# Kernel optimization log

Measured on AMD Instinct MI355X. Metric: run time of the kernel, lower is better.

Reference implementation:

```python
import jax, jax.numpy as jnp
import numpy as np

NUM_HEADS = 8
HEAD_SPLITS = [2, 3, 3]            # heads per crpe window {3:2, 5:3, 7:3}
WINDOWS = [3, 5, 7]


def dwconv(x, w, b, pad):
    """Depthwise conv. x: [B,C,H,W], w: [C,1,kh,kw] (OIHW), b: [C]."""
    y = jax.lax.conv_general_dilated(
        x, w, window_strides=(1, 1), padding=[(pad, pad), (pad, pad)],
        dimension_numbers=("NCHW", "OIHW", "NCHW"),
        feature_group_count=x.shape[1])
    return y + b[None, :, None, None]


def layernorm(x, w, b, eps=1e-6):
    m = jnp.mean(x, axis=-1, keepdims=True)
    v = jnp.mean(jnp.square(x - m), axis=-1, keepdims=True)
    return (x - m) * jax.lax.rsqrt(v + eps) * w + b


def setup_inputs() -> dict:
    key = jax.random.key(0)
    ks = jax.random.split(key, 16)
    B, Hs, Ws, C = 16, 56, 56, 512
    N = Hs * Ws
    Ch = C // NUM_HEADS
    hid = int(C * 4.0)

    def rn(k, shape, s=0.02):
        return jax.random.normal(k, shape, jnp.float32) * s

    return {
        "x": jax.random.normal(ks[0], (B, N, C), jnp.float32),
        "H": Hs, "W": Ws,
        "cpe_w": rn(ks[1], (C, 1, 3, 3)), "cpe_b": jnp.zeros((C,), jnp.float32),
        "ln1_w": jnp.ones((C,), jnp.float32), "ln1_b": jnp.zeros((C,), jnp.float32),
        "qkv_w": rn(ks[2], (C, 3 * C)),
        "proj_w": rn(ks[3], (C, C)), "proj_b": jnp.zeros((C,), jnp.float32),
        "w3": rn(ks[4], (HEAD_SPLITS[0] * Ch, 1, 3, 3)), "b3": jnp.zeros((HEAD_SPLITS[0] * Ch,), jnp.float32),
        "w5": rn(ks[5], (HEAD_SPLITS[1] * Ch, 1, 5, 5)), "b5": jnp.zeros((HEAD_SPLITS[1] * Ch,), jnp.float32),
        "w7": rn(ks[6], (HEAD_SPLITS[2] * Ch, 1, 7, 7)), "b7": jnp.zeros((HEAD_SPLITS[2] * Ch,), jnp.float32),
        "ln2_w": jnp.ones((C,), jnp.float32), "ln2_b": jnp.zeros((C,), jnp.float32),
        "fc1_w": rn(ks[7], (C, hid)), "fc1_b": jnp.zeros((hid,), jnp.float32),
        "fc2_w": rn(ks[8], (hid, C)), "fc2_b": jnp.zeros((C,), jnp.float32),
    }


def reference(x, H, W, cpe_w, cpe_b, ln1_w, ln1_b, qkv_w, proj_w, proj_b,
              w3, b3, w5, b5, w7, b7, ln2_w, ln2_b, fc1_w, fc1_b, fc2_w, fc2_b):
    B, N, C = x.shape
    h = NUM_HEADS
    Ch = C // h
    scale = Ch ** -0.5

    # --- ConvPosEnc (no cls token: N == H*W branch) ---
    feat = jnp.transpose(x, (0, 2, 1)).reshape(B, C, H, W)
    feat = dwconv(feat, cpe_w, cpe_b, pad=1) + feat
    x0 = jnp.transpose(feat.reshape(B, C, N), (0, 2, 1))  # [B,N,C]

    # --- FactorAttnConvRelPosEnc ---
    cur = layernorm(x0, ln1_w, ln1_b)
    qkv = (cur @ qkv_w).reshape(B, N, 3, h, Ch)
    qkv = jnp.transpose(qkv, (2, 0, 3, 1, 4))  # [3,B,h,N,Ch]
    q, k, v = qkv[0], qkv[1], qkv[2]

    k_sm = jax.nn.softmax(k, axis=2)                    # softmax over tokens
    kv = jnp.einsum("bhnk,bhnv->bhkv", k_sm, v)         # [B,h,Ch,Ch]
    factor_att = jnp.einsum("bhnk,bhkv->bhnv", q, kv)   # [B,h,N,Ch]

    # ConvRelPosEnc: grouped depthwise convs on v per head split
    v_img = jnp.transpose(v, (0, 1, 3, 2)).reshape(B, h * Ch, H, W)
    c0, c1 = HEAD_SPLITS[0] * Ch, (HEAD_SPLITS[0] + HEAD_SPLITS[1]) * Ch
    conv_v = jnp.concatenate([
        dwconv(v_img[:, :c0], w3, b3, pad=1),
        dwconv(v_img[:, c0:c1], w5, b5, pad=2),
        dwconv(v_img[:, c1:], w7, b7, pad=3),
    ], axis=1)
    conv_v = jnp.transpose(conv_v.reshape(B, h, Ch, N), (0, 1, 3, 2))  # [B,h,N,Ch]
    crpe = q * conv_v

    attn = scale * factor_att + crpe
    attn = jnp.transpose(attn, (0, 2, 1, 3)).reshape(B, N, C)
    attn = attn @ proj_w + proj_b

    x0 = x0 + attn

    # --- FFN ---
    cur = layernorm(x0, ln2_w, ln2_b)
    hdn = jax.nn.gelu(cur @ fc1_w + fc1_b, approximate=False)
    out = x0 + (hdn @ fc2_w + fc2_b)
    return out
```

## Files before the change

### kernel.cpp

```cpp
#include <hip/hip_runtime.h>
#include <hip/hip_bf16.h>

typedef unsigned short ushort_t;
typedef unsigned int uint_t;

typedef float f32x4 __attribute__((ext_vector_type(4)));
typedef short s16x8 __attribute__((ext_vector_type(8)));

#define HW 56
#define NTOK 3136
#define CDIM 512
#define NHEAD 8
#define CH 64
#define QKVC 1536
#define HID 2048
#define NSEG 28
#define SEGLEN 112

#define WPK_TOTAL 19976

__device__ __forceinline__ float b2f(ushort_t u) {
    union { uint_t i; float f; } cv; cv.i = ((uint_t)u) << 16; return cv.f;
}
__device__ __forceinline__ ushort_t f2b(float f) {
    union { __hip_bfloat16 h; ushort_t u; } cv; cv.h = __float2bfloat16(f); return cv.u;
}
__device__ __forceinline__ uint_t pk2(float a, float b) {
    return (uint_t)f2b(a) | ((uint_t)f2b(b) << 16);
}

__device__ __forceinline__ void gload_lds16(const ushort_t* g, ushort_t* l) {
    __builtin_amdgcn_global_load_lds(
        (const __attribute__((address_space(1))) void*)g,
        (__attribute__((address_space(3))) void*)l, 16, 0, 0);
}

__global__ __launch_bounds__(256) void k_transpose(const float* __restrict__ in,
                                                   ushort_t* __restrict__ out,
                                                   int K, int Npr) {
    __shared__ float tile[32][33];
    int tx = threadIdx.x & 31, ty = threadIdx.x >> 5;
    int kb = blockIdx.y * 32, nb = blockIdx.x * 32;
#pragma unroll
    for (int i = 0; i < 4; i++)
        tile[ty + i * 8][tx] = in[(size_t)(kb + ty + i * 8) * Npr + nb + tx];
    __syncthreads();
#pragma unroll
    for (int i = 0; i < 4; i++)
        out[(size_t)(nb + ty + i * 8) * K + kb + tx] = f2b(tile[tx][ty + i * 8]);
}

__global__ __launch_bounds__(256) void k_wtrans(const float* __restrict__ cpe_w,
                                                const float* __restrict__ w3,
                                                const float* __restrict__ w5,
                                                const float* __restrict__ w7,
                                                float* __restrict__ wpk) {
    int idx = blockIdx.x * 256 + threadIdx.x;
    if (idx < 4608) {
        int i = idx / 512, c = idx % 512;
        wpk[idx] = cpe_w[c * 9 + i];
    } else if (idx < 5760) {
        int r = idx - 4608; int i = r / 128, c = r % 128;
        wpk[idx] = w3[c * 9 + i];
    } else if (idx < 10560) {
        int r = idx - 5760; int i = r / 192, c = r % 192;
        wpk[idx] = w5[c * 25 + i];
    } else if (idx < 19968) {
        int r = idx - 10560; int i = r / 192, c = r % 192;
        wpk[idx] = w7[c * 49 + i];
    } else if (idx < WPK_TOTAL) {
        wpk[idx] = 0.f;
    }
}

__global__ __launch_bounds__(256) void k_cpe(const float* __restrict__ x,
                                             const float* __restrict__ wpk,
                                             const float* __restrict__ bias,
                                             float* __restrict__ x0) {
    int t = threadIdx.x;
    int tok = t >> 7;
    int c0 = (t & 127) * 4;
    int bb = blockIdx.y;
    int n = blockIdx.x * 2 + tok;
    int y = n / HW, xx = n % HW;
    const float* xb = x + ((size_t)bb * NTOK) * CDIM + c0;
    const float* zf = wpk + 19968;
    float4 a = *(const float4*)(bias + c0);
#pragma unroll
    for (int i = 0; i < 9; i++) {
        int ky = i / 3 - 1, kx = i % 3 - 1;
        int yy = y + ky, xc = xx + kx;
        bool ok = (unsigned)yy < HW && (unsigned)xc < HW;
        const float* ap = ok ? (xb + (size_t)(yy * HW + xc) * CDIM) : zf;
        float4 d = *(const float4*)ap;
        float4 w = *(const float4*)(wpk + i * 512 + c0);
        a.x += w.x * d.x; a.y += w.y * d.y; a.z += w.z * d.z; a.w += w.w * d.w;
    }
    float4 ctr = *(const float4*)(xb + (size_t)n * CDIM);
    a.x += ctr.x; a.y += ctr.y; a.z += ctr.z; a.w += ctr.w;
    *(float4*)(x0 + ((size_t)bb * NTOK + n) * CDIM + c0) = a;
}

__global__ __launch_bounds__(256) void k_ln(const float* __restrict__ in,
                                            const float* __restrict__ w,
                                            const float* __restrict__ b,
                                            ushort_t* __restrict__ out) {
    int wid = threadIdx.x >> 6, lane = threadIdx.x & 63;
    size_t row = (size_t)blockIdx.x * 4 + wid;
    const float* p = in + row * CDIM + lane * 8;
    float4 v0 = *(const float4*)p;
    float4 v1 = *(const float4*)(p + 4);
    float v[8] = { v0.x, v0.y, v0.z, v0.w, v1.x, v1.y, v1.z, v1.w };
    float s = 0.f, s2 = 0.f;
#pragma unroll
    for (int i = 0; i < 8; i++) { s += v[i]; s2 += v[i] * v[i]; }
#pragma unroll
    for (int m = 1; m < 64; m <<= 1) { s += __shfl_xor(s, m); s2 += __shfl_xor(s2, m); }
    float mean = s * (1.f / CDIM);
    float var = s2 * (1.f / CDIM) - mean * mean;
    float rstd = rsqrtf(var + 1e-6f);
    float4 w0 = *(const float4*)(w + lane * 8);
    float4 w1 = *(const float4*)(w + lane * 8 + 4);
    float4 b0 = *(const float4*)(b + lane * 8);
    float4 b1 = *(const float4*)(b + lane * 8 + 4);
    float wv[8] = { w0.x, w0.y, w0.z, w0.w, w1.x, w1.y, w1.z, w1.w };
    float bv[8] = { b0.x, b0.y, b0.z, b0.w, b1.x, b1.y, b1.z, b1.w };
    float o[8];
#pragma unroll
    for (int i = 0; i < 8; i++) o[i] = (v[i] - mean) * rstd * wv[i] + bv[i];
    uint4 ro;
    ro.x = pk2(o[0], o[1]); ro.y = pk2(o[2], o[3]); ro.z = pk2(o[4], o[5]); ro.w = pk2(o[6], o[7]);
    *(uint4*)(out + row * CDIM + lane * 8) = ro;
}

template <int EPI>
__global__ __launch_bounds__(256, 3) void k_gemm(const ushort_t* __restrict__ A,
                                                 const ushort_t* __restrict__ Bt,
                                                 const float* __restrict__ bias,
                                                 const float* __restrict__ res,
                                                 void* __restrict__ outv,
                                                 int M, int Npr, int K) {
    __shared__ ushort_t As[128 * 64];
    __shared__ ushort_t Bs[128 * 64];
    int t = threadIdx.x;
    int m0 = blockIdx.y * 128, n0 = blockIdx.x * 128;
    int wid = t >> 6, lane = t & 63, q = lane >> 4, r16 = lane & 15;
    int wr = wid >> 1, wc = wid & 1;
    f32x4 acc[4][4] = {};

    int srow = lane >> 3;
    int scol = ((lane & 7) ^ srow) * 8;
    const ushort_t* pA[4];
    const ushort_t* pB[4];
    int lofs[4];
#pragma unroll
    for (int c = 0; c < 4; c++) {
        int rowc = wid * 32 + c * 8 + srow;
        int ra = m0 + rowc; if (ra > M - 1) ra = M - 1;
        pA[c] = A + (size_t)ra * K + scol;
        pB[c] = Bt + (size_t)(n0 + rowc) * K + scol;
        lofs[c] = (wid * 32 + c * 8) * 64;
    }

    for (int k0 = 0; k0 < K; k0 += 64) {
#pragma unroll
        for (int c = 0; c < 4; c++) gload_lds16(pA[c] + k0, &As[lofs[c]]);
#pragma unroll
        for (int c = 0; c < 4; c++) gload_lds16(pB[c] + k0, &Bs[lofs[c]]);
        __syncthreads();
#pragma unroll
        for (int kk = 0; kk < 64; kk += 32) {
            s16x8 a[4], b[4];
#pragma unroll
            for (int i = 0; i < 4; i++) {
                int R = wr * 64 + i * 16 + r16;
                a[i] = *(const s16x8*)&As[R * 64 + ((kk + q * 8) ^ ((R & 7) * 8))];
            }
#pragma unroll
            for (int j = 0; j < 4; j++) {
                int S = wc * 64 + j * 16 + r16;
                b[j] = *(const s16x8*)&Bs[S * 64 + ((kk + q * 8) ^ ((S & 7) * 8))];
            }
#pragma unroll
            for (int mi = 0; mi < 4; mi++)
#pragma unroll
                for (int ni = 0; ni < 4; ni++)
                    acc[mi][ni] = __builtin_amdgcn_mfma_f32_16x16x32_bf16(a[mi], b[ni], acc[mi][ni], 0, 0, 0);
        }
        __syncthreads();
    }

#pragma unroll
    for (int mi = 0; mi < 4; mi++) {
#pragma unroll
        for (int ni = 0; ni < 4; ni++) {
            int col = n0 + wc * 64 + ni * 16 + r16;
            float bv = 0.f;
            if (EPI != 0) bv = bias[col];
#pragma unroll
            for (int r = 0; r < 4; r++) {
                int row = m0 + wr * 64 + mi * 16 + q * 4 + r;
                if (row >= M) continue;
                float xv = acc[mi][ni][r];
                size_t idx = (size_t)row * Npr + col;
                if (EPI == 0) {
                    ((ushort_t*)outv)[idx] = f2b(xv);
                } else if (EPI == 1) {
                    ((float*)outv)[idx] = xv + bv + res[idx];
                } else {
                    xv += bv;
                    xv = 0.5f * xv * (1.f + erff(xv * 0.70710678118654752f));
                    ((ushort_t*)outv)[idx] = f2b(xv);
                }
            }
        }
    }
}

__global__ __launch_bounds__(256) void k_sm_part(const ushort_t* __restrict__ qkv,
                                                 float* __restrict__ mxp,
                                                 float* __restrict__ ssp) {
    int cblk = blockIdx.x, seg = blockIdx.y, b = blockIdx.z;
    int ch = threadIdx.x & 63, nt = threadIdx.x >> 6;
    int c0 = cblk * 64;
    const ushort_t* base = qkv + (size_t)b * NTOK * QKVC + CDIM + c0 + ch;
    int nbeg = seg * SEGLEN, nend = nbeg + SEGLEN;
    __shared__ float red[4][64];
    float mx = -1e30f;
    for (int n = nbeg + nt; n < nend; n += 4) mx = fmaxf(mx, b2f(base[(size_t)n * QKVC]));
    red[nt][ch] = mx;
    __syncthreads();
    mx = fmaxf(fmaxf(red[0][ch], red[1][ch]), fmaxf(red[2][ch], red[3][ch]));
    __syncthreads();
    float s = 0.f;
    for (int n = nbeg + nt; n < nend; n += 4) s += __expf(b2f(base[(size_t)n * QKVC]) - mx);
    red[nt][ch] = s;
    __syncthreads();
    if (nt == 0) {
        s = red[0][ch] + red[1][ch] + red[2][ch] + red[3][ch];
        size_t o = ((size_t)b * CDIM + c0 + ch) * NSEG + seg;
        mxp[o] = mx;
        ssp[o] = s;
    }
}

__global__ __launch_bounds__(512) void k_sm_red(const float* __restrict__ mxp,
                                                const float* __restrict__ ssp,
                                                float* __restrict__ Mx,
                                                float* __restrict__ Sx) {
    int b = blockIdx.x, c = threadIdx.x;
    const float* mp = mxp + ((size_t)b * CDIM + c) * NSEG;
    const float* sp = ssp + ((size_t)b * CDIM + c) * NSEG;
    float m = -1e30f;
#pragma unroll 4
    for (int s = 0; s < NSEG; s++) m = fmaxf(m, mp[s]);
    float S = 0.f;
#pragma unroll 4
    for (int s = 0; s < NSEG; s++) S += sp[s] * __expf(mp[s] - m);
    Mx[b * CDIM + c] = m;
    Sx[b * CDIM + c] = S;
}

__global__ __launch_bounds__(256) void k_kv_part(const ushort_t* __restrict__ qkv,
                                                 const float* __restrict__ Mx,
                                                 float* __restrict__ kvpart) {
    int hd = blockIdx.x, seg = blockIdx.y, b = blockIdx.z;
    int c0 = hd * CH;
    int t = threadIdx.x, tx = t & 15, ty = t >> 4;
    __shared__ float mx[64];
    __shared__ float ek[8][64];
    __shared__ float vv[8][64];
    if (t < 64) mx[t] = Mx[b * CDIM + c0 + t];
    __syncthreads();
    float acc[4][4] = {};
    const ushort_t* kbase = qkv + (size_t)b * NTOK * QKVC + CDIM + c0;
    const ushort_t* vbase = kbase + CDIM;
    int nbeg = seg * SEGLEN;
    for (int n0 = nbeg; n0 < nbeg + SEGLEN; n0 += 8) {
        for (int idx = t; idx < 512; idx += 256) {
            int r = idx >> 6, ch = idx & 63;
            ek[r][ch] = __expf(b2f(kbase[(size_t)(n0 + r) * QKVC + ch]) - mx[ch]);
            vv[r][ch] = b2f(vbase[(size_t)(n0 + r) * QKVC + ch]);
        }
        __syncthreads();
#pragma unroll
        for (int r = 0; r < 8; r++) {
            float ekv[4], vvv[4];
#pragma unroll
            for (int i = 0; i < 4; i++) ekv[i] = ek[r][ty * 4 + i];
#pragma unroll
            for (int j = 0; j < 4; j++) vvv[j] = vv[r][tx * 4 + j];
#pragma unroll
            for (int i = 0; i < 4; i++)
#pragma unroll
                for (int j = 0; j < 4; j++) acc[i][j] += ekv[i] * vvv[j];
        }
        __syncthreads();
    }
    float* outp = kvpart + (((size_t)(b * NHEAD + hd)) * NSEG + seg) * 4096;
#pragma unroll
    for (int i = 0; i < 4; i++)
#pragma unroll
        for (int j = 0; j < 4; j++)
            outp[(size_t)(ty * 4 + i) * CH + tx * 4 + j] = acc[i][j];
}

__global__ __launch_bounds__(256) void k_kv_red(const float* __restrict__ kvpart,
                                                const float* __restrict__ Sx,
                                                float* __restrict__ kv) {
    int quad = blockIdx.x, hd = blockIdx.y, b = blockIdx.z;
    int bh = b * NHEAD + hd;
    int t = threadIdx.x;
    const float* basep = kvpart + ((size_t)bh * NSEG) * 4096 + quad * 1024;
    const float scale = 0.125f;
#pragma unroll
    for (int k = 0; k < 4; k++) {
        int e = k * 256 + t;
        float s = 0.f;
        for (int sg = 0; sg < NSEG; sg++) s += basep[(size_t)sg * 4096 + e];
        int ck = (quad * 1024 + e) >> 6;
        float sinv = scale / Sx[b * CDIM + hd * CH + ck];
        kv[(size_t)bh * 4096 + quad * 1024 + e] = s * sinv;
    }
}

__global__ __launch_bounds__(256) void k_convv(const ushort_t* __restrict__ qkv,
                                               const float* __restrict__ wpk,
                                               const float* __restrict__ b3,
                                               const float* __restrict__ b5,
                                               const float* __restrict__ b7,
                                               ushort_t* __restrict__ conv) {
    int t = threadIdx.x;
    int wv = t >> 6, lane = t & 63;
    int bb = blockIdx.y;
    int n0 = blockIdx.x * 16 + wv * 4;
    int ch0 = lane * 8;
    int ks, pad, base, stride; const float* bias;
    if (lane < 16)      { ks = 3; pad = 1; base = 4608 + ch0;          stride = 128; bias = b3 + ch0; }
    else if (lane < 40) { ks = 5; pad = 2; base = 5760 + (ch0 - 128);  stride = 192; bias = b5 + (ch0 - 128); }
    else                { ks = 7; pad = 3; base = 10560 + (ch0 - 320); stride = 192; bias = b7 + (ch0 - 320); }
    int ks2 = ks * ks;
    const ushort_t* vb = qkv + (size_t)bb * NTOK * QKVC + 2 * CDIM + ch0;
    const ushort_t* zp = (const ushort_t*)(wpk + 19968);
    float4 blo = *(const float4*)(bias);
    float4 bhi = *(const float4*)(bias + 4);
    float acc[4][8];
    int ty[4], txx[4];
#pragma unroll
    for (int k4 = 0; k4 < 4; k4++) {
        int n = n0 + k4; ty[k4] = n / HW; txx[k4] = n % HW;
        acc[k4][0] = blo.x; acc[k4][1] = blo.y; acc[k4][2] = blo.z; acc[k4][3] = blo.w;
        acc[k4][4] = bhi.x; acc[k4][5] = bhi.y; acc[k4][6] = bhi.z; acc[k4][7] = bhi.w;
    }
    int ky = -pad, kx = -pad;
    for (int i = 0; i < 49; i++) {
        bool act = i < ks2;
        int ie = act ? i : 0;
        const float* wp = wpk + base + ie * stride;
        float4 wlo = *(const float4*)wp;
        float4 whi = *(const float4*)(wp + 4);
        float w[8] = { wlo.x, wlo.y, wlo.z, wlo.w, whi.x, whi.y, whi.z, whi.w };
#pragma unroll
        for (int k4 = 0; k4 < 4; k4++) {
            int yy = ty[k4] + ky, xc = txx[k4] + kx;
            bool ok = act && (unsigned)yy < HW && (unsigned)xc < HW;
            const ushort_t* ap = ok ? (vb + (size_t)(yy * HW + xc) * QKVC) : zp;
            uint4 d = *(const uint4*)ap;
            float dv[8];
            dv[0] = b2f(d.x & 0xffff); dv[1] = b2f(d.x >> 16);
            dv[2] = b2f(d.y & 0xffff); dv[3] = b2f(d.y >> 16);
            dv[4] = b2f(d.z & 0xffff); dv[5] = b2f(d.z >> 16);
            dv[6] = b2f(d.w & 0xffff); dv[7] = b2f(d.w >> 16);
#pragma unroll
            for (int j = 0; j < 8; j++) acc[k4][j] += w[j] * dv[j];
        }
        kx++; if (kx > pad) { kx = -pad; ky++; }
    }
#pragma unroll
    for (int k4 = 0; k4 < 4; k4++) {
        int n = n0 + k4;
        uint4 o;
        o.x = pk2(acc[k4][0], acc[k4][1]);
        o.y = pk2(acc[k4][2], acc[k4][3]);
        o.z = pk2(acc[k4][4], acc[k4][5]);
        o.w = pk2(acc[k4][6], acc[k4][7]);
        *(uint4*)&conv[((size_t)bb * NTOK + n) * CDIM + ch0] = o;
    }
}

__global__ __launch_bounds__(256) void k_attn(const ushort_t* __restrict__ qkv,
                                              const float* __restrict__ kv,
                                              ushort_t* __restrict__ conv) {
    int nb = blockIdx.x, hd = blockIdx.y, b = blockIdx.z;
    int t = threadIdx.x, tx = t & 15, ty = t >> 4;
    __shared__ float kvl[64 * 64];
    __shared__ float ql[64 * 65];
    const float* kvsrc = kv + (size_t)(b * NHEAD + hd) * CH * CH;
    for (int idx = t; idx < 4096; idx += 256) kvl[idx] = kvsrc[idx];
    const ushort_t* qbase = qkv + ((size_t)b * NTOK + nb * 64) * QKVC + hd * CH;
    for (int idx = t; idx < 4096; idx += 256) {
        int r = idx >> 6, ck = idx & 63;
        ql[r * 65 + ck] = b2f(qbase[(size_t)r * QKVC + ck]);
    }
    __syncthreads();
    float acc[4][4] = {};
    for (int ck = 0; ck < 64; ck++) {
        float kvr[4];
#pragma unroll
        for (int j = 0; j < 4; j++) kvr[j] = kvl[ck * 64 + tx * 4 + j];
#pragma unroll
        for (int i = 0; i < 4; i++) {
            float qv = ql[(ty + 16 * i) * 65 + ck];
#pragma unroll
            for (int j = 0; j < 4; j++) acc[i][j] += qv * kvr[j];
        }
    }
    size_t obase = (size_t)b * NTOK + nb * 64;
#pragma unroll
    for (int i = 0; i < 4; i++) {
        int row = ty + 16 * i;
        size_t o = (obase + row) * CDIM + hd * CH + tx * 4;
        uint2 cv = *(const uint2*)&conv[o];
        float c0 = b2f((ushort_t)(cv.x & 0xffff)), c1 = b2f((ushort_t)(cv.x >> 16));
        float c2 = b2f((ushort_t)(cv.y & 0xffff)), c3 = b2f((ushort_t)(cv.y >> 16));
        float q0 = ql[row * 65 + tx * 4 + 0];
        float q1 = ql[row * 65 + tx * 4 + 1];
        float q2 = ql[row * 65 + tx * 4 + 2];
        float q3 = ql[row * 65 + tx * 4 + 3];
        uint2 ov;
        ov.x = pk2(acc[i][0] + q0 * c0, acc[i][1] + q1 * c1);
        ov.y = pk2(acc[i][2] + q2 * c2, acc[i][3] + q3 * c3);
        *(uint2*)&conv[o] = ov;
    }
}

extern "C" void kernel_launch(void* const* d_in, const int* in_sizes, int n_in,
                              void* d_out, int out_size, void* d_ws, size_t ws_size,
                              hipStream_t stream) {
    const float* x     = (const float*)d_in[0];
    const float* cpe_w = (const float*)d_in[3];
    const float* cpe_b = (const float*)d_in[4];
    const float* ln1_w = (const float*)d_in[5];
    const float* ln1_b = (const float*)d_in[6];
    const float* qkv_w = (const float*)d_in[7];
    const float* proj_w = (const float*)d_in[8];
    const float* proj_b = (const float*)d_in[9];
    const float* w3 = (const float*)d_in[10];
    const float* b3 = (const float*)d_in[11];
    const float* w5 = (const float*)d_in[12];
    const float* b5 = (const float*)d_in[13];
    const float* w7 = (const float*)d_in[14];
    const float* b7 = (const float*)d_in[15];
    const float* ln2_w = (const float*)d_in[16];
    const float* ln2_b = (const float*)d_in[17];
    const float* fc1_w = (const float*)d_in[18];
    const float* fc1_b = (const float*)d_in[19];
    const float* fc2_w = (const float*)d_in[20];
    const float* fc2_b = (const float*)d_in[21];
    float* out = (float*)d_out;

    char* p = (char*)d_ws;
    ushort_t* wt_qkv  = (ushort_t*)p; p += (size_t)QKVC * CDIM * 2;
    ushort_t* wt_proj = (ushort_t*)p; p += (size_t)CDIM * CDIM * 2;
    ushort_t* wt_fc1  = (ushort_t*)p; p += (size_t)HID * CDIM * 2;
    ushort_t* wt_fc2  = (ushort_t*)p; p += (size_t)CDIM * HID * 2;
    float* wpk = (float*)p; p += 20480 * 4;
    size_t wt_bytes = (size_t)(p - (char*)d_ws);

    k_transpose<<<dim3(QKVC / 32, CDIM / 32), 256, 0, stream>>>(qkv_w, wt_qkv, CDIM, QKVC);
    k_transpose<<<dim3(CDIM / 32, CDIM / 32), 256, 0, stream>>>(proj_w, wt_proj, CDIM, CDIM);
    k_transpose<<<dim3(HID / 32, CDIM / 32), 256, 0, stream>>>(fc1_w, wt_fc1, CDIM, HID);
    k_transpose<<<dim3(CDIM / 32, HID / 32), 256, 0, stream>>>(fc2_w, wt_fc2, HID, CDIM);
    k_wtrans<<<(WPK_TOTAL + 255) / 256, 256, 0, stream>>>(cpe_w, w3, w5, w7, wpk);

    const size_t per_b = (size_t)NTOK * CDIM * 2
                       + (size_t)NTOK * HID * 2
                       + (size_t)NHEAD * CH * CH * 4
                       + (size_t)NHEAD * NSEG * 4096 * 4
                       + (size_t)CDIM * 4 * 2
                       + (size_t)CDIM * NSEG * 4 * 2;
    int Bc = 16;
    while (Bc > 1 && wt_bytes + (size_t)Bc * per_b > ws_size) Bc >>= 1;

    ushort_t* cur = (ushort_t*)p; p += (size_t)Bc * NTOK * CDIM * 2;
    char* un = p;                 p += (size_t)Bc * NTOK * HID * 2;
    ushort_t* conv = (ushort_t*)un;
    ushort_t* qkvb = (ushort_t*)(un + (size_t)Bc * NTOK * CDIM * 2);
    ushort_t* hid  = (ushort_t*)un;
    float* kvb    = (float*)p; p += (size_t)Bc * NHEAD * CH * CH * 4;
    float* kvpart = (float*)p; p += (size_t)Bc * NHEAD * NSEG * 4096 * 4;
    float* Mx  = (float*)p; p += (size_t)Bc * CDIM * 4;
    float* Sx  = (float*)p; p += (size_t)Bc * CDIM * 4;
    float* mxp = (float*)p; p += (size_t)Bc * CDIM * NSEG * 4;
    float* ssp = (float*)p;

    for (int b0 = 0; b0 < 16; b0 += Bc) {
        int M = Bc * NTOK;
        int gy = (M + 127) / 128;
        const float* xch = x + (size_t)b0 * NTOK * CDIM;
        float* och = out + (size_t)b0 * NTOK * CDIM;
        float* x0 = och;

        k_cpe<<<dim3(NTOK / 2, Bc), 256, 0, stream>>>(xch, wpk, cpe_b, x0);
        k_ln<<<M / 4, 256, 0, stream>>>(x0, ln1_w, ln1_b, cur);
        k_gemm<0><<<dim3(QKVC / 128, gy), 256, 0, stream>>>(cur, wt_qkv, nullptr, nullptr, qkvb, M, QKVC, CDIM);
        k_sm_part<<<dim3(8, NSEG, Bc), 256, 0, stream>>>(qkvb, mxp, ssp);
        k_sm_red<<<Bc, 512, 0, stream>>>(mxp, ssp, Mx, Sx);
        k_kv_part<<<dim3(NHEAD, NSEG, Bc), 256, 0, stream>>>(qkvb, Mx, kvpart);
        k_kv_red<<<dim3(4, NHEAD, Bc), 256, 0, stream>>>(kvpart, Sx, kvb);
        k_convv<<<dim3(NTOK / 16, Bc), 256, 0, stream>>>(qkvb, wpk, b3, b5, b7, conv);
        k_attn<<<dim3(NTOK / 64, NHEAD, Bc), 256, 0, stream>>>(qkvb, kvb, conv);
        k_gemm<1><<<dim3(CDIM / 128, gy), 256, 0, stream>>>(conv, wt_proj, proj_b, x0, x0, M, CDIM, CDIM);
        k_ln<<<M / 4, 256, 0, stream>>>(x0, ln2_w, ln2_b, cur);
        k_gemm<2><<<dim3(HID / 128, gy), 256, 0, stream>>>(cur, wt_fc1, fc1_b, nullptr, hid, M, HID, CDIM);
        k_gemm<1><<<dim3(CDIM / 128, gy), 256, 0, stream>>>(hid, wt_fc2, fc2_b, x0, och, M, CDIM, HID);
    }
}
```

Baseline: 1.271 ms.

## Double-buffer LDS tiles in GEMM to overlap global loads with MFMA

The GEMM kernel now uses two LDS buffers per operand. The next K-tile is issued with direct global-to-LDS loads while MFMAs run on the current tile, with an explicit vmcnt wait plus barrier between stages. This is meant to hide global load latency that the single-buffer loop exposed between its two syncthreads. In exchange LDS use doubles to 64KB per block and launch bounds drop from 3 to 2 blocks per CU, which lowers occupancy. The loop assumes K is a multiple of 128.

Result: slower. 1.473 ms (+15.8%).

```diff
diff --git a/kernel.cpp b/kernel.cpp
--- a/kernel.cpp
+++ b/kernel.cpp
@@ -134,19 +134,22 @@
 }
 
 template <int EPI>
-__global__ __launch_bounds__(256, 3) void k_gemm(const ushort_t* __restrict__ A,
+__global__ __launch_bounds__(256, 2) void k_gemm(const ushort_t* __restrict__ A,
                                                  const ushort_t* __restrict__ Bt,
                                                  const float* __restrict__ bias,
                                                  const float* __restrict__ res,
                                                  void* __restrict__ outv,
                                                  int M, int Npr, int K) {
-    __shared__ ushort_t As[128 * 64];
-    __shared__ ushort_t Bs[128 * 64];
+    __shared__ ushort_t As0[128 * 64];
+    __shared__ ushort_t Bs0[128 * 64];
+    __shared__ ushort_t As1[128 * 64];
+    __shared__ ushort_t Bs1[128 * 64];
     int t = threadIdx.x;
     int m0 = blockIdx.y * 128, n0 = blockIdx.x * 128;
     int wid = t >> 6, lane = t & 63, q = lane >> 4, r16 = lane & 15;
     int wr = wid >> 1, wc = wid & 1;
     f32x4 acc[4][4] = {};
+    s16x8 a[4], bfr[4];
 
     int srow = lane >> 3;
     int scol = ((lane & 7) ^ srow) * 8;
@@ -162,33 +165,46 @@
         lofs[c] = (wid * 32 + c * 8) * 64;
     }
 
-    for (int k0 = 0; k0 < K; k0 += 64) {
-#pragma unroll
-        for (int c = 0; c < 4; c++) gload_lds16(pA[c] + k0, &As[lofs[c]]);
-#pragma unroll
-        for (int c = 0; c < 4; c++) gload_lds16(pB[c] + k0, &Bs[lofs[c]]);
-        __syncthreads();
-#pragma unroll
-        for (int kk = 0; kk < 64; kk += 32) {
-            s16x8 a[4], b[4];
-#pragma unroll
-            for (int i = 0; i < 4; i++) {
-                int R = wr * 64 + i * 16 + r16;
-                a[i] = *(const s16x8*)&As[R * 64 + ((kk + q * 8) ^ ((R & 7) * 8))];
-            }
-#pragma unroll
-            for (int j = 0; j < 4; j++) {
-                int S = wc * 64 + j * 16 + r16;
-                b[j] = *(const s16x8*)&Bs[S * 64 + ((kk + q * 8) ^ ((S & 7) * 8))];
-            }
-#pragma unroll
-            for (int mi = 0; mi < 4; mi++)
-#pragma unroll
-                for (int ni = 0; ni < 4; ni++)
-                    acc[mi][ni] = __builtin_amdgcn_mfma_f32_16x16x32_bf16(a[mi], b[ni], acc[mi][ni], 0, 0, 0);
-        }
-        __syncthreads();
-    }
+#define STAGE(AS, BS, kn) do {                                                  \
+    _Pragma("unroll") for (int c = 0; c < 4; c++) gload_lds16(pA[c] + (kn), &AS[lofs[c]]); \
+    _Pragma("unroll") for (int c = 0; c < 4; c++) gload_lds16(pB[c] + (kn), &BS[lofs[c]]); \
+} while (0)
+
+#define COMPUTE(AS, BS) do {                                                    \
+    _Pragma("unroll") for (int kk = 0; kk < 64; kk += 32) {                     \
+        _Pragma("unroll") for (int i = 0; i < 4; i++) {                         \
+            int R = wr * 64 + i * 16 + r16;                                     \
+            a[i] = *(const s16x8*)&AS[R * 64 + ((kk + q * 8) ^ ((R & 7) * 8))]; \
+        }                                                                       \
+        _Pragma("unroll") for (int j = 0; j < 4; j++) {                         \
+            int S = wc * 64 + j * 16 + r16;                                     \
+            bfr[j] = *(const s16x8*)&BS[S * 64 + ((kk + q * 8) ^ ((S & 7) * 8))]; \
+        }                                                                       \
+        _Pragma("unroll") for (int mi = 0; mi < 4; mi++)                        \
+        _Pragma("unroll") for (int ni = 0; ni < 4; ni++)                        \
+            acc[mi][ni] = __builtin_amdgcn_mfma_f32_16x16x32_bf16(a[mi], bfr[ni], acc[mi][ni], 0, 0, 0); \
+    }                                                                           \
+} while (0)
+
+#define DRAIN_BAR() do {                                                        \
+    asm volatile("s_waitcnt vmcnt(0)" ::: "memory");                            \
+    __builtin_amdgcn_s_barrier();                                               \
+} while (0)
+
+    STAGE(As0, Bs0, 0);
+
+    for (int k0 = 0; k0 < K; k0 += 128) {
+        DRAIN_BAR();
+        STAGE(As1, Bs1, k0 + 64);
+        COMPUTE(As0, Bs0);
+        DRAIN_BAR();
+        if (k0 + 128 < K) STAGE(As0, Bs0, k0 + 128);
+        COMPUTE(As1, Bs1);
+    }
+
+#undef STAGE
+#undef COMPUTE
+#undef DRAIN_BAR
 
 #pragma unroll
     for (int mi = 0; mi < 4; mi++) {
```
